# Optimization experiments

Hardware: AMD Instinct MI355X
Metric: run time of the kernel (lower is better)

## Reference

```python
import jax, jax.numpy as jnp
import numpy as np

B, S, BD, AD, H, NITER = 16, 512, 768, 768, 12, 3  # batch, seq, bert_dim, attention_dim, heads, c_c_Attention_num
DH = AD // H
SCALE = float(np.sqrt(BD))  # note: original scales by sqrt(bert_dim), not head dim


def setup_inputs() -> dict:
    key = jax.random.key(0)
    ks = jax.random.split(key, 12)
    sd = 0.02
    return {
        "sequence1": jax.random.normal(ks[0], (B, S, BD), dtype=jnp.float32),
        "sequence2": jax.random.normal(ks[1], (B, S, BD), dtype=jnp.float32),
        # first-layer projections (bias=False), torch Linear weight layout [out, in]
        "Wq": jax.random.normal(ks[2], (AD, BD), dtype=jnp.float32) * sd,
        "Wk": jax.random.normal(ks[3], (AD, BD), dtype=jnp.float32) * sd,
        "Wv": jax.random.normal(ks[4], (AD, BD), dtype=jnp.float32) * sd,
        # later-layer projections (with bias), stacked over layer_num-1 = 2 layers
        "Wq1": jax.random.normal(ks[5], (2, AD, AD), dtype=jnp.float32) * sd,
        "bq1": jax.random.normal(ks[6], (2, AD), dtype=jnp.float32) * sd,
        "Wk1": jax.random.normal(ks[7], (2, AD, AD), dtype=jnp.float32) * sd,
        "bk1": jax.random.normal(ks[8], (2, AD), dtype=jnp.float32) * sd,
        "Wv1": jax.random.normal(ks[9], (2, AD, AD), dtype=jnp.float32) * sd,
        "bv1": jax.random.normal(ks[10], (2, AD), dtype=jnp.float32) * sd,
    }


def _attention(s1, s2, Wq, bq, Wk, bk, Wv, bv):
    # dropout is identity in eval mode
    q = s1 @ Wq.T + bq  # [B,S,AD]
    k = s2 @ Wk.T + bk
    v = s2 @ Wv.T + bv
    # torch.split along feature dim then stack on dim 0 == reshape to heads
    qh = q.reshape(B, S, H, DH)
    kh = k.reshape(B, S, H, DH)
    vh = v.reshape(B, S, H, DH)
    scores = jnp.einsum("bqhd,bkhd->hbqk", qh, kh)  # [H,B,S,S]
    scores = jax.nn.softmax(jnp.tanh(scores) / SCALE, axis=3)
    ctx = jnp.einsum("hbqk,bkhd->bqhd", scores, vh).reshape(B, S, AD)
    return ctx, scores


def reference(sequence1, sequence2, Wq, Wk, Wv, Wq1, bq1, Wk1, bk1, Wv1, bv1):
    s1, s2 = sequence1, sequence2
    ctx, sc = None, None
    for i in range(NITER):
        if i == 0:
            ctx, sc = _attention(s1, s2, Wq, 0.0, Wk, 0.0, Wv, 0.0)
        else:
            j = i - 1
            ctx, sc = _attention(s1, s2, Wq1[j], bq1[j], Wk1[j], bk1[j], Wv1[j], bv1[j])
        s1 = ctx
        s2 = ctx
    return ctx, ctx, sc
```

## Files before the change

### kernel.cpp

```cpp
#include <hip/hip_runtime.h>
#include <stdint.h>

typedef unsigned short u16;
typedef unsigned int u32;

typedef __bf16 bf16x8 __attribute__((ext_vector_type(8)));
typedef float f32x4 __attribute__((ext_vector_type(4)));

#define NQ 6291456
#define NW 589824
#define INV_SCALE 0.03608439182435161f

__device__ __forceinline__ u16 f2bf(float f) {
    u32 u = __float_as_uint(f);
    u32 r = (u + 0x7fffu + ((u >> 16) & 1u)) >> 16;
    return (u16)r;
}

__device__ __forceinline__ void gload_lds16(const void* g, void* l) {
    __builtin_amdgcn_global_load_lds(
        (const __attribute__((address_space(1))) char*)(uintptr_t)g,
        (__attribute__((address_space(3))) char*)(uintptr_t)l, 16, 0, 0);
}

__device__ __forceinline__ f32x4 mfma16(bf16x8 a, bf16x8 b, f32x4 c) {
    return __builtin_amdgcn_mfma_f32_16x16x32_bf16(a, b, c, 0, 0, 0);
}

__global__ __launch_bounds__(256) void cvt(const float* __restrict__ s,
                                           u16* __restrict__ d, int n4)
{
    int i = blockIdx.x * 256 + threadIdx.x;
    if (i < n4) {
        float4 v = ((const float4*)s)[i];
        ushort4 o;
        o.x = f2bf(v.x); o.y = f2bf(v.y); o.z = f2bf(v.z); o.w = f2bf(v.w);
        ((ushort4*)d)[i] = o;
    }
}

__global__ __launch_bounds__(256, 2) void proj_gemm(
    const u16* __restrict__ A0, const u16* __restrict__ A1,
    const u16* __restrict__ Wq, const u16* __restrict__ Wk, const u16* __restrict__ Wv,
    const float* __restrict__ bq, const float* __restrict__ bk, const float* __restrict__ bv,
    u16* __restrict__ oq, u16* __restrict__ ok, u16* __restrict__ ov)
{
    __shared__ u16 sA[8192];
    __shared__ u16 sB[8192];

    const int z = blockIdx.z;
    const u16* A       = (z == 0) ? A0 : A1;
    const u16* W       = (z == 0) ? Wq : ((z == 1) ? Wk : Wv);
    const float* bias  = (z == 0) ? bq : ((z == 1) ? bk : bv);
    u16* out           = (z == 0) ? oq : ((z == 1) ? ok : ov);

    const int tid = threadIdx.x;
    const int wave = tid >> 6, lane = tid & 63;
    const int m0 = blockIdx.x * 128, n0 = blockIdx.y * 128;
    const int wrow = wave >> 1, wcol = wave & 1;
    const int lr = lane & 15, lg = lane >> 4;

    f32x4 acc[4][4];
#pragma unroll
    for (int mi = 0; mi < 4; ++mi)
#pragma unroll
        for (int ni = 0; ni < 4; ++ni)
            acc[mi][ni] = (f32x4){0.f, 0.f, 0.f, 0.f};

    for (int ks = 0; ks < 12; ++ks) {
        const int k0 = ks * 64;
#pragma unroll
        for (int i = 0; i < 4; ++i) {
            const int Lb = wave * 4096 + i * 1024;
            const int L = Lb + lane * 16;
            const int row = L >> 7;
            const int sc16 = (lane & 7) ^ (row & 7);
            gload_lds16(A + (size_t)(m0 + row) * 768 + k0 + sc16 * 8, (char*)sA + Lb);
            gload_lds16(W + (size_t)(n0 + row) * 768 + k0 + sc16 * 8, (char*)sB + Lb);
        }
        __syncthreads();
#pragma unroll
        for (int kk = 0; kk < 2; ++kk) {
            bf16x8 af[4], bfr[4];
#pragma unroll
            for (int t = 0; t < 4; ++t) {
                const int ar = wrow * 64 + t * 16 + lr;
                const int ac = (kk * 4 + lg) ^ (ar & 7);
                af[t] = *(const bf16x8*)((const char*)sA + ar * 128 + ac * 16);
                const int br = wcol * 64 + t * 16 + lr;
                const int bc = (kk * 4 + lg) ^ (br & 7);
                bfr[t] = *(const bf16x8*)((const char*)sB + br * 128 + bc * 16);
            }
#pragma unroll
            for (int mi = 0; mi < 4; ++mi)
#pragma unroll
                for (int ni = 0; ni < 4; ++ni)
                    acc[mi][ni] = mfma16(af[mi], bfr[ni], acc[mi][ni]);
        }
        __syncthreads();
    }

    float bvv[4] = {0.f, 0.f, 0.f, 0.f};
    if (bias) {
#pragma unroll
        for (int ni = 0; ni < 4; ++ni)
            bvv[ni] = bias[n0 + wcol * 64 + ni * 16 + lr];
    }
#pragma unroll
    for (int mi = 0; mi < 4; ++mi) {
#pragma unroll
        for (int ni = 0; ni < 4; ++ni) {
#pragma unroll
            for (int r = 0; r < 4; ++r) {
                const int rowM = m0 + wrow * 64 + mi * 16 + lg * 4 + r;
                const int colN = n0 + wcol * 64 + ni * 16 + lr;
                out[(size_t)rowM * 768 + colN] = f2bf(acc[mi][ni][r] + bvv[ni]);
            }
        }
    }
}

__global__ __launch_bounds__(256) void vtrans(const u16* __restrict__ v, u16* __restrict__ vT)
{
    __shared__ u16 t[64][80];
    const int blk = blockIdx.x;
    const int b = blk / 96, h = (blk / 8) % 12, st = blk & 7;
    const int tid = threadIdx.x;

    const u16* src = v + (size_t)(b * 512 + st * 64) * 768 + h * 64;
#pragma unroll
    for (int p = 0; p < 2; ++p) {
        const int srow = p * 32 + (tid >> 3), dp = tid & 7;
        uint4 d = *(const uint4*)(src + (size_t)srow * 768 + dp * 8);
        *(uint4*)&t[srow][dp * 8] = d;
    }
    __syncthreads();
    u16* dst = vT + (size_t)((b * 12 + h) * 64) * 512 + st * 64;
#pragma unroll
    for (int p = 0; p < 2; ++p) {
        const int drow = p * 32 + (tid >> 3), sp = tid & 7;
        union { u16 u[8]; uint4 v4; } o;
#pragma unroll
        for (int j = 0; j < 8; ++j) o.u[j] = t[sp * 8 + j][drow];
        *(uint4*)(dst + (size_t)drow * 512 + sp * 8) = o.v4;
    }
}

template <bool FINAL>
__global__ __launch_bounds__(256, 2) void attn_kernel(
    const u16* __restrict__ q, const u16* __restrict__ k, const u16* __restrict__ vT,
    u16* __restrict__ ctxb, float* __restrict__ ctxf, float* __restrict__ sc)
{
    __shared__ u16 sP[4][8192];
    __shared__ float ssum[4][16];

    const int blk = blockIdx.x;
    const int b = blk / 96, h = (blk / 8) % 12, qc = blk & 7;
    const int tid = threadIdx.x, wave = tid >> 6, lane = tid & 63;
    const int q0 = qc * 64 + wave * 16;
    const int lr = lane & 15, lg = lane >> 4;
    char* myP = (char*)sP[wave];

    const u16* qbase = q + (size_t)(b * 512 + q0 + lr) * 768 + h * 64 + lg * 8;
    bf16x8 aq0 = *(const bf16x8*)(qbase);
    bf16x8 aq1 = *(const bf16x8*)(qbase + 32);

    float psum[4] = {0.f, 0.f, 0.f, 0.f};
    const u16* kbase = k + (size_t)(b * 512 + lr) * 768 + h * 64 + lg * 8;

    for (int kt = 0; kt < 32; ++kt) {
        f32x4 s4 = (f32x4){0.f, 0.f, 0.f, 0.f};
        const u16* kb = kbase + (size_t)kt * 16 * 768;
        s4 = mfma16(aq0, *(const bf16x8*)kb, s4);
        s4 = mfma16(aq1, *(const bf16x8*)(kb + 32), s4);
#pragma unroll
        for (int r = 0; r < 4; ++r) {
            const int row = lg * 4 + r;
            float e = __expf(2.f * s4[r]);
            float th = 1.f - __fdividef(2.f, e + 1.f);
            float p = __expf(th * INV_SCALE);
            psum[r] += p;
            const int byte = (row * 1024 + (kt * 16 + lr) * 2) ^ ((row & 7) << 4);
            *(u16*)(myP + byte) = f2bf(p);
        }
    }
#pragma unroll
    for (int r = 0; r < 4; ++r) {
        psum[r] += __shfl_xor(psum[r], 1);
        psum[r] += __shfl_xor(psum[r], 2);
        psum[r] += __shfl_xor(psum[r], 4);
        psum[r] += __shfl_xor(psum[r], 8);
    }
    float inv[4];
#pragma unroll
    for (int r = 0; r < 4; ++r) inv[r] = 1.f / psum[r];

    if (FINAL && lr == 0) {
#pragma unroll
        for (int r = 0; r < 4; ++r) ssum[wave][lg * 4 + r] = inv[r];
    }

    const u16* vb0 = vT + (size_t)((b * 12 + h) * 64 + lr) * 512 + lg * 8;
#pragma unroll
    for (int dt = 0; dt < 4; ++dt) {
        f32x4 o = (f32x4){0.f, 0.f, 0.f, 0.f};
        const u16* vbb = vb0 + (size_t)dt * 16 * 512;
#pragma unroll
        for (int pk = 0; pk < 16; ++pk) {
            const int byte = (lr * 1024 + pk * 64 + lg * 16) ^ ((lr & 7) << 4);
            bf16x8 pa = *(const bf16x8*)(myP + byte);
            bf16x8 vb = *(const bf16x8*)(vbb + pk * 32);
            o = mfma16(pa, vb, o);
        }
#pragma unroll
        for (int r = 0; r < 4; ++r) {
            const int rowq = lg * 4 + r;
            const float val = o[r] * inv[r];
            const size_t gi = (size_t)(b * 512 + q0 + rowq) * 768 + h * 64 + dt * 16 + lr;
            if (FINAL) {
                ctxf[gi] = val;
                ctxf[gi + (size_t)NQ] = val;
            } else {
                ctxb[gi] = f2bf(val);
            }
        }
    }

    if (FINAL) {
#pragma unroll
        for (int row = 0; row < 16; ++row) {
            const float is = ssum[wave][row];
            const int byte = (row * 1024 + lane * 16) ^ ((row & 7) << 4);
            bf16x8 pv8 = *(const bf16x8*)(myP + byte);
            float4 o0, o1;
            o0.x = (float)pv8[0] * is; o0.y = (float)pv8[1] * is;
            o0.z = (float)pv8[2] * is; o0.w = (float)pv8[3] * is;
            o1.x = (float)pv8[4] * is; o1.y = (float)pv8[5] * is;
            o1.z = (float)pv8[6] * is; o1.w = (float)pv8[7] * is;
            float* dstp = sc + ((size_t)((h * 16 + b) * 512 + q0 + row)) * 512 + lane * 8;
            *(float4*)dstp = o0;
            *(float4*)(dstp + 4) = o1;
        }
    }
}

extern "C" void kernel_launch(void* const* d_in, const int* in_sizes, int n_in,
                              void* d_out, int out_size, void* d_ws, size_t ws_size,
                              hipStream_t stream)
{
    if (n_in < 11) return;
    const float* seq1 = (const float*)d_in[0];
    const float* seq2 = (const float*)d_in[1];
    const float* Wq  = (const float*)d_in[2];
    const float* Wk  = (const float*)d_in[3];
    const float* Wv  = (const float*)d_in[4];
    const float* Wq1 = (const float*)d_in[5];
    const float* bq1 = (const float*)d_in[6];
    const float* Wk1 = (const float*)d_in[7];
    const float* bk1 = (const float*)d_in[8];
    const float* Wv1 = (const float*)d_in[9];
    const float* bv1 = (const float*)d_in[10];

    if (ws_size < ((size_t)7 * NQ + 9 * NW) * 2) return;
    u16* ws   = (u16*)d_ws;
    u16* q    = ws;
    u16* kk   = ws + (size_t)NQ;
    u16* vv   = ws + (size_t)2 * NQ;
    u16* vT   = ws + (size_t)3 * NQ;
    u16* ctx  = ws + (size_t)4 * NQ;
    u16* bs1  = ws + (size_t)5 * NQ;
    u16* bs2  = ws + (size_t)6 * NQ;
    u16* bWq  = ws + (size_t)7 * NQ;
    u16* bWk  = bWq  + (size_t)NW;
    u16* bWv  = bWk  + (size_t)NW;
    u16* bWq1 = bWv  + (size_t)NW;
    u16* bWk1 = bWq1 + (size_t)2 * NW;
    u16* bWv1 = bWk1 + (size_t)2 * NW;

    float* out = (float*)d_out;

    cvt<<<6144, 256, 0, stream>>>(seq1, bs1, NQ / 4);
    cvt<<<6144, 256, 0, stream>>>(seq2, bs2, NQ / 4);
    cvt<<<576, 256, 0, stream>>>(Wq, bWq, NW / 4);
    cvt<<<576, 256, 0, stream>>>(Wk, bWk, NW / 4);
    cvt<<<576, 256, 0, stream>>>(Wv, bWv, NW / 4);
    cvt<<<1152, 256, 0, stream>>>(Wq1, bWq1, NW / 2);
    cvt<<<1152, 256, 0, stream>>>(Wk1, bWk1, NW / 2);
    cvt<<<1152, 256, 0, stream>>>(Wv1, bWv1, NW / 2);

    dim3 pgrid(64, 6, 3);

    proj_gemm<<<pgrid, 256, 0, stream>>>(bs1, bs2, bWq, bWk, bWv,
                                         nullptr, nullptr, nullptr, q, kk, vv);
    vtrans<<<1536, 256, 0, stream>>>(vv, vT);
    attn_kernel<false><<<1536, 256, 0, stream>>>(q, kk, vT, ctx, nullptr, nullptr);

    proj_gemm<<<pgrid, 256, 0, stream>>>(ctx, ctx, bWq1, bWk1, bWv1,
                                         bq1, bk1, bv1, q, kk, vv);
    vtrans<<<1536, 256, 0, stream>>>(vv, vT);
    attn_kernel<false><<<1536, 256, 0, stream>>>(q, kk, vT, ctx, nullptr, nullptr);

    proj_gemm<<<pgrid, 256, 0, stream>>>(ctx, ctx, bWq1 + (size_t)NW, bWk1 + (size_t)NW,
                                         bWv1 + (size_t)NW,
                                         bq1 + 768, bk1 + 768, bv1 + 768, q, kk, vv);
    vtrans<<<1536, 256, 0, stream>>>(vv, vT);
    attn_kernel<true><<<1536, 256, 0, stream>>>(q, kk, vT, nullptr, out,
                                                out + (size_t)2 * NQ);
}
```

Baseline: 488.6 us.

## Fuse conversions, double-buffer projection GEMM, stream attention for intermediate layers

Merges the eight fp32-to-bf16 conversion launches into one multi-segment kernel. Double-buffers the projection GEMM's LDS tiles so the next K-slice loads while the current one computes. Adds a streaming attention kernel for the non-final layers that processes keys 32 at a time through a small per-wave LDS buffer, letting it run at higher occupancy than the full 16x512 probability tile. Replaces the second exp with a cubic Taylor polynomial, which is only accurate because tanh/sqrt(768) keeps the argument small.

```diff
diff --git a/kernel.cpp b/kernel.cpp
--- a/kernel.cpp
+++ b/kernel.cpp
@@ -10,6 +10,7 @@
 #define NQ 6291456
 #define NW 589824
 #define INV_SCALE 0.03608439182435161f
+#define LOG2E2 2.885390081777927f
 
 __device__ __forceinline__ u16 f2bf(float f) {
     u32 u = __float_as_uint(f);
@@ -17,6 +18,13 @@
     return (u16)r;
 }
 
+__device__ __forceinline__ float score_p(float s) {
+    float e  = exp2f(LOG2E2 * s);
+    float th = 1.f - __fdividef(2.f, e + 1.f);
+    float a  = th * INV_SCALE;
+    return fmaf(a, fmaf(a, fmaf(a, 0.16666667f, 0.5f), 1.f), 1.f);
+}
+
 __device__ __forceinline__ void gload_lds16(const void* g, void* l) {
     __builtin_amdgcn_global_load_lds(
         (const __attribute__((address_space(1))) char*)(uintptr_t)g,
@@ -27,15 +35,27 @@
     return __builtin_amdgcn_mfma_f32_16x16x32_bf16(a, b, c, 0, 0, 0);
 }
 
-__global__ __launch_bounds__(256) void cvt(const float* __restrict__ s,
-                                           u16* __restrict__ d, int n4)
-{
-    int i = blockIdx.x * 256 + threadIdx.x;
-    if (i < n4) {
-        float4 v = ((const float4*)s)[i];
+#define LDS_FENCE() asm volatile("s_waitcnt lgkmcnt(0)" ::: "memory")
+
+struct CvtArgs {
+    const float* src[8];
+    u16* dst[8];
+    int blk_start[8];
+    int n4[8];
+};
+
+__global__ __launch_bounds__(256) void cvt_multi(CvtArgs a)
+{
+    const int bid = blockIdx.x;
+    int seg = 0;
+#pragma unroll
+    for (int s = 1; s < 8; ++s) seg += (bid >= a.blk_start[s]);
+    const int i = (bid - a.blk_start[seg]) * 256 + threadIdx.x;
+    if (i < a.n4[seg]) {
+        float4 v = ((const float4*)a.src[seg])[i];
         ushort4 o;
         o.x = f2bf(v.x); o.y = f2bf(v.y); o.z = f2bf(v.z); o.w = f2bf(v.w);
-        ((ushort4*)d)[i] = o;
+        ((ushort4*)a.dst[seg])[i] = o;
     }
 }
 
@@ -45,8 +65,8 @@
     const float* __restrict__ bq, const float* __restrict__ bk, const float* __restrict__ bv,
     u16* __restrict__ oq, u16* __restrict__ ok, u16* __restrict__ ov)
 {
-    __shared__ u16 sA[8192];
-    __shared__ u16 sB[8192];
+    __shared__ u16 sA[2][8192];
+    __shared__ u16 sB[2][8192];
 
     const int z = blockIdx.z;
     const u16* A       = (z == 0) ? A0 : A1;
@@ -60,6 +80,10 @@
     const int wrow = wave >> 1, wcol = wave & 1;
     const int lr = lane & 15, lg = lane >> 4;
 
+    const int Lb0 = wave * 4096;
+    const int srow = (Lb0 + lane * 16) >> 7;
+    const int ssl = (lane & 7);
+
     f32x4 acc[4][4];
 #pragma unroll
     for (int mi = 0; mi < 4; ++mi)
@@ -67,18 +91,25 @@
         for (int ni = 0; ni < 4; ++ni)
             acc[mi][ni] = (f32x4){0.f, 0.f, 0.f, 0.f};
 
+#define STAGE(buf, k0)                                                          \
+    {                                                                           \
+        _Pragma("unroll")                                                       \
+        for (int i = 0; i < 4; ++i) {                                           \
+            const int row = srow + i * 8;                                       \
+            const int sc16 = ssl ^ (row & 7);                                   \
+            gload_lds16(A + (size_t)(m0 + row) * 768 + (k0) + sc16 * 8,         \
+                        (char*)sA[buf] + Lb0 + i * 1024);                       \
+            gload_lds16(W + (size_t)(n0 + row) * 768 + (k0) + sc16 * 8,         \
+                        (char*)sB[buf] + Lb0 + i * 1024);                       \
+        }                                                                       \
+    }
+
+    STAGE(0, 0);
+    __syncthreads();
+
     for (int ks = 0; ks < 12; ++ks) {
-        const int k0 = ks * 64;
-#pragma unroll
-        for (int i = 0; i < 4; ++i) {
-            const int Lb = wave * 4096 + i * 1024;
-            const int L = Lb + lane * 16;
-            const int row = L >> 7;
-            const int sc16 = (lane & 7) ^ (row & 7);
-            gload_lds16(A + (size_t)(m0 + row) * 768 + k0 + sc16 * 8, (char*)sA + Lb);
-            gload_lds16(W + (size_t)(n0 + row) * 768 + k0 + sc16 * 8, (char*)sB + Lb);
-        }
-        __syncthreads();
+        const int cur = ks & 1;
+        if (ks < 11) STAGE(cur ^ 1, (ks + 1) * 64);
 #pragma unroll
         for (int kk = 0; kk < 2; ++kk) {
             bf16x8 af[4], bfr[4];
@@ -86,10 +117,10 @@
             for (int t = 0; t < 4; ++t) {
                 const int ar = wrow * 64 + t * 16 + lr;
                 const int ac = (kk * 4 + lg) ^ (ar & 7);
-                af[t] = *(const bf16x8*)((const char*)sA + ar * 128 + ac * 16);
+                af[t] = *(const bf16x8*)((const char*)sA[cur] + ar * 128 + ac * 16);
                 const int br = wcol * 64 + t * 16 + lr;
                 const int bc = (kk * 4 + lg) ^ (br & 7);
-                bfr[t] = *(const bf16x8*)((const char*)sB + br * 128 + bc * 16);
+                bfr[t] = *(const bf16x8*)((const char*)sB[cur] + br * 128 + bc * 16);
             }
 #pragma unroll
             for (int mi = 0; mi < 4; ++mi)
@@ -99,6 +130,7 @@
         }
         __syncthreads();
     }
+#undef STAGE
 
     float bvv[4] = {0.f, 0.f, 0.f, 0.f};
     if (bias) {
@@ -146,10 +178,89 @@
     }
 }
 
-template <bool FINAL>
-__global__ __launch_bounds__(256, 2) void attn_kernel(
+__global__ __launch_bounds__(256, 4) void attn_stream(
     const u16* __restrict__ q, const u16* __restrict__ k, const u16* __restrict__ vT,
-    u16* __restrict__ ctxb, float* __restrict__ ctxf, float* __restrict__ sc)
+    u16* __restrict__ ctx)
+{
+    __shared__ u16 sS[4][2][640];
+
+    const int blk = blockIdx.x;
+    const int b = blk / 96, h = (blk / 8) % 12, qc = blk & 7;
+    const int tid = threadIdx.x, wave = tid >> 6, lane = tid & 63;
+    const int q0 = qc * 64 + wave * 16;
+    const int lr = lane & 15, lg = lane >> 4;
+
+    const u16* qbase = q + (size_t)(b * 512 + q0 + lr) * 768 + h * 64 + lg * 8;
+    bf16x8 aq0 = *(const bf16x8*)(qbase);
+    bf16x8 aq1 = *(const bf16x8*)(qbase + 32);
+
+    const u16* kbase = k + (size_t)(b * 512 + lr) * 768 + h * 64 + lg * 8;
+    const u16* vbase = vT + (size_t)((b * 12 + h) * 64 + lr) * 512 + lg * 8;
+
+    char* const myS0 = (char*)sS[wave][0];
+    const int rdoff = lr * 80 + ((lg * 16) ^ ((lr & 3) << 4));
+
+    float psum[4] = {0.f, 0.f, 0.f, 0.f};
+    f32x4 o[4];
+#pragma unroll
+    for (int dt = 0; dt < 4; ++dt) o[dt] = (f32x4){0.f, 0.f, 0.f, 0.f};
+
+    for (int w = 0; w < 16; ++w) {
+        char* myS = myS0 + (w & 1) * 1280;
+        const u16* kb = kbase + (size_t)w * 32 * 768;
+        f32x4 s4a = (f32x4){0.f, 0.f, 0.f, 0.f};
+        f32x4 s4b = (f32x4){0.f, 0.f, 0.f, 0.f};
+        s4a = mfma16(aq0, *(const bf16x8*)kb, s4a);
+        s4a = mfma16(aq1, *(const bf16x8*)(kb + 32), s4a);
+        const u16* kb2 = kb + 16 * 768;
+        s4b = mfma16(aq0, *(const bf16x8*)kb2, s4b);
+        s4b = mfma16(aq1, *(const bf16x8*)(kb2 + 32), s4b);
+
+#pragma unroll
+        for (int c = 0; c < 2; ++c) {
+#pragma unroll
+            for (int r = 0; r < 4; ++r) {
+                const float s = c ? s4b[r] : s4a[r];
+                const float p = score_p(s);
+                psum[r] += p;
+                const int row = lg * 4 + r;
+                const int byte = row * 80 + (((c * 16 + lr) * 2) ^ ((r & 3) << 4));
+                *(u16*)(myS + byte) = f2bf(p);
+            }
+        }
+        LDS_FENCE();
+        bf16x8 pa = *(const bf16x8*)(myS + rdoff);
+#pragma unroll
+        for (int dt = 0; dt < 4; ++dt) {
+            bf16x8 vb = *(const bf16x8*)(vbase + (size_t)dt * 16 * 512 + w * 32);
+            o[dt] = mfma16(pa, vb, o[dt]);
+        }
+    }
+
+#pragma unroll
+    for (int r = 0; r < 4; ++r) {
+        psum[r] += __shfl_xor(psum[r], 1);
+        psum[r] += __shfl_xor(psum[r], 2);
+        psum[r] += __shfl_xor(psum[r], 4);
+        psum[r] += __shfl_xor(psum[r], 8);
+    }
+    float inv[4];
+#pragma unroll
+    for (int r = 0; r < 4; ++r) inv[r] = 1.f / psum[r];
+
+#pragma unroll
+    for (int dt = 0; dt < 4; ++dt) {
+#pragma unroll
+        for (int r = 0; r < 4; ++r) {
+            const size_t gi = (size_t)(b * 512 + q0 + lg * 4 + r) * 768 + h * 64 + dt * 16 + lr;
+            ctx[gi] = f2bf(o[dt][r] * inv[r]);
+        }
+    }
+}
+
+__global__ __launch_bounds__(256, 2) void attn_final(
+    const u16* __restrict__ q, const u16* __restrict__ k, const u16* __restrict__ vT,
+    float* __restrict__ ctxf, float* __restrict__ sc)
 {
     __shared__ u16 sP[4][8192];
     __shared__ float ssum[4][16];
@@ -176,9 +287,7 @@
 #pragma unroll
         for (int r = 0; r < 4; ++r) {
             const int row = lg * 4 + r;
-            float e = __expf(2.f * s4[r]);
-            float th = 1.f - __fdividef(2.f, e + 1.f);
-            float p = __expf(th * INV_SCALE);
+            const float p = score_p(s4[r]);
             psum[r] += p;
             const int byte = (row * 1024 + (kt * 16 + lr) * 2) ^ ((row & 7) << 4);
             *(u16*)(myP + byte) = f2bf(p);
@@ -195,7 +304,7 @@
 #pragma unroll
     for (int r = 0; r < 4; ++r) inv[r] = 1.f / psum[r];
 
-    if (FINAL && lr == 0) {
+    if (lr == 0) {
 #pragma unroll
         for (int r = 0; r < 4; ++r) ssum[wave][lg * 4 + r] = inv[r];
     }
@@ -214,33 +323,26 @@
         }
 #pragma unroll
         for (int r = 0; r < 4; ++r) {
-            const int rowq = lg * 4 + r;
             const float val = o[r] * inv[r];
-            const size_t gi = (size_t)(b * 512 + q0 + rowq) * 768 + h * 64 + dt * 16 + lr;
-            if (FINAL) {
-                ctxf[gi] = val;
-                ctxf[gi + (size_t)NQ] = val;
-            } else {
-                ctxb[gi] = f2bf(val);
-            }
-        }
-    }
-
-    if (FINAL) {
-#pragma unroll
-        for (int row = 0; row < 16; ++row) {
-            const float is = ssum[wave][row];
-            const int byte = (row * 1024 + lane * 16) ^ ((row & 7) << 4);
-            bf16x8 pv8 = *(const bf16x8*)(myP + byte);
-            float4 o0, o1;
-            o0.x = (float)pv8[0] * is; o0.y = (float)pv8[1] * is;
-            o0.z = (float)pv8[2] * is; o0.w = (float)pv8[3] * is;
-            o1.x = (float)pv8[4] * is; o1.y = (float)pv8[5] * is;
-            o1.z = (float)pv8[6] * is; o1.w = (float)pv8[7] * is;
-            float* dstp = sc + ((size_t)((h * 16 + b) * 512 + q0 + row)) * 512 + lane * 8;
-            *(float4*)dstp = o0;
-            *(float4*)(dstp + 4) = o1;
-        }
+            const size_t gi = (size_t)(b * 512 + q0 + lg * 4 + r) * 768 + h * 64 + dt * 16 + lr;
+            ctxf[gi] = val;
+            ctxf[gi + (size_t)NQ] = val;
+        }
+    }
+
+#pragma unroll
+    for (int row = 0; row < 16; ++row) {
+        const float is = ssum[wave][row];
+        const int byte = (row * 1024 + lane * 16) ^ ((row & 7) << 4);
+        bf16x8 pv8 = *(const bf16x8*)(myP + byte);
+        float4 o0, o1;
+        o0.x = (float)pv8[0] * is; o0.y = (float)pv8[1] * is;
+        o0.z = (float)pv8[2] * is; o0.w = (float)pv8[3] * is;
+        o1.x = (float)pv8[4] * is; o1.y = (float)pv8[5] * is;
+        o1.z = (float)pv8[6] * is; o1.w = (float)pv8[7] * is;
+        float* dstp = sc + ((size_t)((h * 16 + b) * 512 + q0 + row)) * 512 + lane * 8;
+        *(float4*)dstp = o0;
+        *(float4*)(dstp + 4) = o1;
     }
 }
 
@@ -279,31 +381,33 @@
 
     float* out = (float*)d_out;
 
-    cvt<<<6144, 256, 0, stream>>>(seq1, bs1, NQ / 4);
-    cvt<<<6144, 256, 0, stream>>>(seq2, bs2, NQ / 4);
-    cvt<<<576, 256, 0, stream>>>(Wq, bWq, NW / 4);
-    cvt<<<576, 256, 0, stream>>>(Wk, bWk, NW / 4);
-    cvt<<<576, 256, 0, stream>>>(Wv, bWv, NW / 4);
-    cvt<<<1152, 256, 0, stream>>>(Wq1, bWq1, NW / 2);
-    cvt<<<1152, 256, 0, stream>>>(Wk1, bWk1, NW / 2);
-    cvt<<<1152, 256, 0, stream>>>(Wv1, bWv1, NW / 2);
+    CvtArgs ca;
+    const float* srcs[8] = {seq1, seq2, Wq, Wk, Wv, Wq1, Wk1, Wv1};
+    u16* dsts[8] = {bs1, bs2, bWq, bWk, bWv, bWq1, bWk1, bWv1};
+    const int n4s[8] = {NQ/4, NQ/4, NW/4, NW/4, NW/4, NW/2, NW/2, NW/2};
+    int acc_blk = 0;
+    for (int s = 0; s < 8; ++s) {
+        ca.src[s] = srcs[s]; ca.dst[s] = dsts[s]; ca.n4[s] = n4s[s];
+        ca.blk_start[s] = acc_blk;
+        acc_blk += (n4s[s] + 255) / 256;
+    }
+    cvt_multi<<<acc_blk, 256, 0, stream>>>(ca);
 
     dim3 pgrid(64, 6, 3);
 
     proj_gemm<<<pgrid, 256, 0, stream>>>(bs1, bs2, bWq, bWk, bWv,
                                          nullptr, nullptr, nullptr, q, kk, vv);
     vtrans<<<1536, 256, 0, stream>>>(vv, vT);
-    attn_kernel<false><<<1536, 256, 0, stream>>>(q, kk, vT, ctx, nullptr, nullptr);
+    attn_stream<<<1536, 256, 0, stream>>>(q, kk, vT, ctx);
 
     proj_gemm<<<pgrid, 256, 0, stream>>>(ctx, ctx, bWq1, bWk1, bWv1,
                                          bq1, bk1, bv1, q, kk, vv);
     vtrans<<<1536, 256, 0, stream>>>(vv, vT);
-    attn_kernel<false><<<1536, 256, 0, stream>>>(q, kk, vT, ctx, nullptr, nullptr);
+    attn_stream<<<1536, 256, 0, stream>>>(q, kk, vT, ctx);
 
     proj_gemm<<<pgrid, 256, 0, stream>>>(ctx, ctx, bWq1 + (size_t)NW, bWk1 + (size_t)NW,
                                          bWv1 + (size_t)NW,
                                          bq1 + 768, bk1 + 768, bv1 + 768, q, kk, vv);
     vtrans<<<1536, 256, 0, stream>>>(vv, vT);
-    attn_kernel<true><<<1536, 256, 0, stream>>>(q, kk, vT, nullptr, out,
-                                                out + (size_t)2 * NQ);
-}
+    attn_final<<<1536, 256, 0, stream>>>(q, kk, vT, out, out + (size_t)2 * NQ);
+}
```

After: 452.6 us. -7.4%, faster.
